# Kernel tuning notes

Hardware: AMD Instinct MI355X
Metric: run time of the kernel (lower is better)

## Reference

```python
import jax, jax.numpy as jnp
import numpy as np

N = 2_000_000   # active voxels
CIN = 16
COUT = 32
K2 = 9          # 3x3 kernel offsets


def setup_inputs() -> dict:
    key = jax.random.key(0)
    ks = jax.random.split(key, 6)
    x = jax.random.normal(ks[0], (N, CIN), dtype=jnp.float32)
    # per-offset neighbor map: nbr_idx[k, i] = input voxel feeding output i at offset k
    nbr_idx = jax.random.randint(ks[1], (K2, N), 0, N, dtype=jnp.int32)
    nbr_mask = jax.random.uniform(ks[2], (K2, N)) < 0.85
    # center offset is always the voxel itself and always valid
    nbr_idx = nbr_idx.at[K2 // 2].set(jnp.arange(N, dtype=jnp.int32))
    nbr_mask = nbr_mask.at[K2 // 2].set(True)
    s1 = 1.0 / np.sqrt(K2 * CIN)
    s2 = 1.0 / np.sqrt(K2 * COUT)
    sp = 1.0 / np.sqrt(CIN)
    W1 = jax.random.uniform(ks[3], (K2, CIN, COUT), jnp.float32, -s1, s1)
    b1 = jnp.zeros((COUT,), jnp.float32)
    W2 = jax.random.uniform(ks[4], (K2, COUT, COUT), jnp.float32, -s2, s2)
    b2 = jnp.zeros((COUT,), jnp.float32)
    Wp = jax.random.uniform(ks[5], (CIN, COUT), jnp.float32, -sp, sp)
    bp = jnp.zeros((COUT,), jnp.float32)
    return {"x": x, "W1": W1, "b1": b1, "W2": W2, "b2": b2,
            "Wp": Wp, "bp": bp, "nbr_idx": nbr_idx, "nbr_mask": nbr_mask}


def _sparse_conv(feats, W, b, nbr_idx, nbr_mask):
    """Gather-GEMM-accumulate sparse conv.
    feats: [N, Cin]; W: [K2, Cin, Cout]; nbr_idx/nbr_mask: [K2, N].
    Scans over the K2 kernel offsets so only one [N, Cin] gather lives at a time.
    """
    acc0 = jnp.zeros((feats.shape[0], W.shape[-1]), feats.dtype)

    def step(acc, kin):
        idx, m, Wk = kin
        g = feats[idx] * m[:, None].astype(feats.dtype)  # masked gather [N, Cin]
        return acc + g @ Wk, None

    acc, _ = jax.lax.scan(step, acc0, (nbr_idx, nbr_mask, W))
    return acc + b


def reference(x, W1, b1, W2, b2, Wp, bp, nbr_idx, nbr_mask):
    h = jax.nn.relu(_sparse_conv(x, W1, b1, nbr_idx, nbr_mask))
    h = _sparse_conv(h, W2, b2, nbr_idx, nbr_mask)
    identity = x @ Wp + bp  # 1x1 sparse projection (in_ch != out_ch)
    return jax.nn.relu(h + identity)
```

## Files before the change

kernel.cpp:

```cpp
#include <hip/hip_runtime.h>
#include <stdint.h>

#define CIN  16
#define COUT 32
#define K2   9

typedef __attribute__((ext_vector_type(8)))  short bf16x8;
typedef __attribute__((ext_vector_type(16))) float f32x16;
typedef __attribute__((ext_vector_type(4)))  float f32x4;

__device__ __forceinline__ uint16_t f2bf(float f) {
    union { float f; uint32_t u; } a; a.f = f;
    uint32_t u = a.u;
    uint32_t r = u + 0x7FFFu + ((u >> 16) & 1u);
    return (uint16_t)(r >> 16);
}
__device__ __forceinline__ float bf2f(uint32_t b16) {
    union { uint32_t u; float f; } a; a.u = b16 << 16; return a.f;
}

__global__ void detect_mask_kernel(const uint32_t* __restrict__ mw,
                                   int* __restrict__ flag,
                                   float* __restrict__ zrow, int n) {
    int t = threadIdx.x;
    uint32_t w = mw[(size_t)4 * (size_t)n + (size_t)t];
    unsigned long long b = __ballot(w == 1u);
    if (t == 0) *flag = (b == ~0ull) ? 1 : 0;
    if (t < 16) zrow[t] = 0.0f;
}

__device__ __forceinline__ bf16x8 make_bfrag(const float* __restrict__ W,
                                             int chbase, int col, int half) {
    bf16x8 f;
    #pragma unroll
    for (int e = 0; e < 8; ++e)
        f[e] = (short)f2bf(W[(chbase + half * 8 + e) * COUT + col]);
    return f;
}

__global__ void __launch_bounds__(256, 4)
conv1_kernel(const float* __restrict__ x,
             const float* __restrict__ W1,
             const float* __restrict__ b1,
             const int*   __restrict__ nidx,
             const void*  __restrict__ nmask,
             const int*   __restrict__ mflag,
             const char*  __restrict__ zrow,
             uint16_t*    __restrict__ hbuf,
             int n)
{
    const int lane = threadIdx.x & 63;
    const int wid  = threadIdx.x >> 6;
    const int col  = lane & 31;
    const int half = lane >> 5;
    const int mode32 = *mflag;
    const int*     m32 = (const int*)nmask;
    const uint8_t* m8  = (const uint8_t*)nmask;

    bf16x8 Bf[K2];
    #pragma unroll
    for (int k = 0; k < K2; ++k)
        Bf[k] = make_bfrag(W1 + k * (CIN * COUT), 0, col, half);
    const float bias = b1[col];

    const int ntiles = (n + 31) >> 5;
    for (int tile = blockIdx.x * 4 + wid; tile < ntiles; tile += gridDim.x * 4) {
        const int vbase = tile << 5;
        const int vr = vbase + col;
        const int vc = (vr < n) ? vr : (n - 1);

        int idv[K2];
        uint32_t mb = 0;
        #pragma unroll
        for (int k = 0; k < K2; ++k) {
            const size_t e = (size_t)k * (size_t)n + (size_t)vc;
            idv[k] = __builtin_nontemporal_load(nidx + e);
            const int m = mode32 ? (__builtin_nontemporal_load(m32 + e) != 0)
                                 : (__builtin_nontemporal_load(m8  + e) != 0);
            mb |= (uint32_t)m << k;
        }

        f32x16 acc = {};

        f32x4 xa = {}, xb = {}, xa1 = {}, xb1 = {};
        {
            const float* p = (mb & 1u)
                ? (x + (size_t)(uint32_t)idv[0] * CIN + half * 8)
                : (const float*)(zrow + half * 32);
            xa = ((const f32x4*)p)[0];
            xb = ((const f32x4*)p)[1];
        }
        #pragma unroll
        for (int k = 0; k < K2; ++k) {
            if (k + 1 < K2) {
                const float* p = ((mb >> (k + 1)) & 1u)
                    ? (x + (size_t)(uint32_t)idv[k + 1] * CIN + half * 8)
                    : (const float*)(zrow + half * 32);
                xa1 = ((const f32x4*)p)[0];
                xb1 = ((const f32x4*)p)[1];
            }
            bf16x8 hi, lo;
            #pragma unroll
            for (int e = 0; e < 8; ++e) {
                const float xv = (e < 4) ? xa[e] : xb[e - 4];
                const uint16_t hb = f2bf(xv);
                hi[e] = (short)hb;
                lo[e] = (short)f2bf(xv - bf2f(hb));
            }
            acc = __builtin_amdgcn_mfma_f32_32x32x16_bf16(hi, Bf[k], acc, 0, 0, 0);
            acc = __builtin_amdgcn_mfma_f32_32x32x16_bf16(lo, Bf[k], acc, 0, 0, 0);
            xa = xa1; xb = xb1;
        }

        #pragma unroll
        for (int r = 0; r < 16; ++r) {
            const int row = (r & 3) + 8 * (r >> 2) + 4 * half;
            const int vo = vbase + row;
            if (vo < n) {
                const float o = fmaxf(acc[r] + bias, 0.0f);
                hbuf[(size_t)vo * COUT + col] = f2bf(o);
            }
        }
    }
}

__global__ void __launch_bounds__(256, 3)
conv2_kernel(const float* __restrict__ x,
             const float* __restrict__ W2,
             const float* __restrict__ b2,
             const float* __restrict__ Wp,
             const float* __restrict__ bp,
             const int*   __restrict__ nidx,
             const void*  __restrict__ nmask,
             const int*   __restrict__ mflag,
             const char*  __restrict__ zrow,
             const uint16_t* __restrict__ hbuf,
             float*       __restrict__ out,
             int n)
{
    const int lane = threadIdx.x & 63;
    const int wid  = threadIdx.x >> 6;
    const int col  = lane & 31;
    const int half = lane >> 5;
    const int mode32 = *mflag;
    const int*     m32 = (const int*)nmask;
    const uint8_t* m8  = (const uint8_t*)nmask;

    bf16x8 Bf0[K2], Bf1[K2];
    #pragma unroll
    for (int k = 0; k < K2; ++k) {
        Bf0[k] = make_bfrag(W2 + k * (COUT * COUT), 0,  col, half);
        Bf1[k] = make_bfrag(W2 + k * (COUT * COUT), 16, col, half);
    }
    const bf16x8 Bp = make_bfrag(Wp, 0, col, half);
    const float bias = b2[col] + bp[col];

    const int ntiles = (n + 31) >> 5;
    for (int tile = blockIdx.x * 4 + wid; tile < ntiles; tile += gridDim.x * 4) {
        const int vbase = tile << 5;
        const int vr = vbase + col;
        const int vc = (vr < n) ? vr : (n - 1);

        int idv[K2];
        uint32_t mb = 0;
        #pragma unroll
        for (int k = 0; k < K2; ++k) {
            const size_t e = (size_t)k * (size_t)n + (size_t)vc;
            idv[k] = __builtin_nontemporal_load(nidx + e);
            const int m = mode32 ? (__builtin_nontemporal_load(m32 + e) != 0)
                                 : (__builtin_nontemporal_load(m8  + e) != 0);
            mb |= (uint32_t)m << k;
        }

        f32x16 acc = {};

        {
            const f32x4* xr = (const f32x4*)(x + (size_t)vc * CIN + half * 8);
            const f32x4 xa = __builtin_nontemporal_load(xr);
            const f32x4 xb = __builtin_nontemporal_load(xr + 1);
            bf16x8 hi, lo;
            #pragma unroll
            for (int e = 0; e < 8; ++e) {
                const float xv = (e < 4) ? xa[e] : xb[e - 4];
                const uint16_t hb = f2bf(xv);
                hi[e] = (short)hb;
                lo[e] = (short)f2bf(xv - bf2f(hb));
            }
            acc = __builtin_amdgcn_mfma_f32_32x32x16_bf16(hi, Bp, acc, 0, 0, 0);
            acc = __builtin_amdgcn_mfma_f32_32x32x16_bf16(lo, Bp, acc, 0, 0, 0);
        }

        bf16x8 A0, A1, N0 = {}, N1 = {};
        {
            const char* p = (mb & 1u)
                ? (const char*)hbuf + (size_t)(uint32_t)idv[0] * (COUT * 2)
                : zrow;
            A0 = *(const bf16x8*)(p + half * 16);
            A1 = *(const bf16x8*)(p + 32 + half * 16);
        }
        #pragma unroll
        for (int k = 0; k < K2; ++k) {
            if (k + 1 < K2) {
                const char* p = ((mb >> (k + 1)) & 1u)
                    ? (const char*)hbuf + (size_t)(uint32_t)idv[k + 1] * (COUT * 2)
                    : zrow;
                N0 = *(const bf16x8*)(p + half * 16);
                N1 = *(const bf16x8*)(p + 32 + half * 16);
            }
            acc = __builtin_amdgcn_mfma_f32_32x32x16_bf16(A0, Bf0[k], acc, 0, 0, 0);
            acc = __builtin_amdgcn_mfma_f32_32x32x16_bf16(A1, Bf1[k], acc, 0, 0, 0);
            A0 = N0; A1 = N1;
        }

        #pragma unroll
        for (int r = 0; r < 16; ++r) {
            const int row = (r & 3) + 8 * (r >> 2) + 4 * half;
            const int vo = vbase + row;
            if (vo < n) {
                const float o = fmaxf(acc[r] + bias, 0.0f);
                __builtin_nontemporal_store(o, out + (size_t)vo * COUT + col);
            }
        }
    }
}

extern "C" void kernel_launch(void* const* d_in, const int* in_sizes, int n_in,
                              void* d_out, int out_size, void* d_ws, size_t ws_size,
                              hipStream_t stream) {
    const float* x    = (const float*)d_in[0];
    const float* W1   = (const float*)d_in[1];
    const float* b1   = (const float*)d_in[2];
    const float* W2   = (const float*)d_in[3];
    const float* b2   = (const float*)d_in[4];
    const float* Wp   = (const float*)d_in[5];
    const float* bp   = (const float*)d_in[6];
    const int*   nidx = (const int*)d_in[7];
    const void*  nmask = d_in[8];
    const int n = in_sizes[0] / CIN;

    int*      mflag = (int*)d_ws;
    float*    zrowf = (float*)((char*)d_ws + 64);
    uint16_t* hbuf  = (uint16_t*)((char*)d_ws + 256);

    detect_mask_kernel<<<1, 64, 0, stream>>>((const uint32_t*)nmask, mflag, zrowf, n);

    const int ntiles = (n + 31) / 32;
    int grid = (ntiles + 3) / 4;
    if (grid > 1024) grid = 1024;

    conv1_kernel<<<grid, 256, 0, stream>>>(x, W1, b1, nidx, nmask, mflag,
                                           (const char*)zrowf, hbuf, n);
    conv2_kernel<<<grid, 256, 0, stream>>>(x, W2, b2, Wp, bp, nidx, nmask, mflag,
                                           (const char*)zrowf, hbuf, (float*)d_out, n);
}
```

Baseline: 1.078 ms.

## Stage weights in LDS and issue all neighbor gathers up front

Weight fragments move from per-thread registers into shared memory, converted to bf16 once per block. This frees VGPRs so conv2 can raise its occupancy bound from 3 to 4 waves, and the grid cap doubles. Both kernels now issue all nine neighbor gathers before any MFMA instead of prefetching one offset ahead, which puts more memory loads in flight to hide the latency of random gathers. The cost is an LDS read per MFMA, more registers to hold the gathered rows, and a per-block weight staging pass.

```diff
diff --git a/kernel.cpp b/kernel.cpp
--- a/kernel.cpp
+++ b/kernel.cpp
@@ -27,15 +27,6 @@
     unsigned long long b = __ballot(w == 1u);
     if (t == 0) *flag = (b == ~0ull) ? 1 : 0;
     if (t < 16) zrow[t] = 0.0f;
-}
-
-__device__ __forceinline__ bf16x8 make_bfrag(const float* __restrict__ W,
-                                             int chbase, int col, int half) {
-    bf16x8 f;
-    #pragma unroll
-    for (int e = 0; e < 8; ++e)
-        f[e] = (short)f2bf(W[(chbase + half * 8 + e) * COUT + col]);
-    return f;
 }
 
 __global__ void __launch_bounds__(256, 4)
@@ -49,6 +40,14 @@
              uint16_t*    __restrict__ hbuf,
              int n)
 {
+    __shared__ __align__(16) uint16_t smw[K2 * 2 * 32 * 8];
+
+    for (int i = threadIdx.x; i < K2 * 2 * 32 * 8; i += 256) {
+        const int e = i & 7, c2 = (i >> 3) & 31, hf = (i >> 8) & 1, k = i >> 9;
+        smw[i] = f2bf(W1[k * (CIN * COUT) + (hf * 8 + e) * COUT + c2]);
+    }
+    __syncthreads();
+
     const int lane = threadIdx.x & 63;
     const int wid  = threadIdx.x >> 6;
     const int col  = lane & 31;
@@ -57,13 +56,9 @@
     const int*     m32 = (const int*)nmask;
     const uint8_t* m8  = (const uint8_t*)nmask;
 
-    bf16x8 Bf[K2];
-    #pragma unroll
-    for (int k = 0; k < K2; ++k)
-        Bf[k] = make_bfrag(W1 + k * (CIN * COUT), 0, col, half);
     const float bias = b1[col];
-
     const int ntiles = (n + 31) >> 5;
+
     for (int tile = blockIdx.x * 4 + wid; tile < ntiles; tile += gridDim.x * 4) {
         const int vbase = tile << 5;
         const int vr = vbase + col;
@@ -80,36 +75,30 @@
             mb |= (uint32_t)m << k;
         }
 
+        f32x4 ga[K2], gb[K2];
+        #pragma unroll
+        for (int k = 0; k < K2; ++k) {
+            const float* p = ((mb >> k) & 1u)
+                ? (x + (size_t)(uint32_t)idv[k] * CIN + half * 8)
+                : (const float*)(zrow + half * 32);
+            ga[k] = ((const f32x4*)p)[0];
+            gb[k] = ((const f32x4*)p)[1];
+        }
+
         f32x16 acc = {};
-
-        f32x4 xa = {}, xb = {}, xa1 = {}, xb1 = {};
-        {
-            const float* p = (mb & 1u)
-                ? (x + (size_t)(uint32_t)idv[0] * CIN + half * 8)
-                : (const float*)(zrow + half * 32);
-            xa = ((const f32x4*)p)[0];
-            xb = ((const f32x4*)p)[1];
-        }
-        #pragma unroll
-        for (int k = 0; k < K2; ++k) {
-            if (k + 1 < K2) {
-                const float* p = ((mb >> (k + 1)) & 1u)
-                    ? (x + (size_t)(uint32_t)idv[k + 1] * CIN + half * 8)
-                    : (const float*)(zrow + half * 32);
-                xa1 = ((const f32x4*)p)[0];
-                xb1 = ((const f32x4*)p)[1];
-            }
+        #pragma unroll
+        for (int k = 0; k < K2; ++k) {
+            const bf16x8 Bf = *(const bf16x8*)&smw[((k * 2 + half) * 32 + col) * 8];
             bf16x8 hi, lo;
             #pragma unroll
             for (int e = 0; e < 8; ++e) {
-                const float xv = (e < 4) ? xa[e] : xb[e - 4];
+                const float xv = (e < 4) ? ga[k][e] : gb[k][e - 4];
                 const uint16_t hb = f2bf(xv);
                 hi[e] = (short)hb;
                 lo[e] = (short)f2bf(xv - bf2f(hb));
             }
-            acc = __builtin_amdgcn_mfma_f32_32x32x16_bf16(hi, Bf[k], acc, 0, 0, 0);
-            acc = __builtin_amdgcn_mfma_f32_32x32x16_bf16(lo, Bf[k], acc, 0, 0, 0);
-            xa = xa1; xb = xb1;
+            acc = __builtin_amdgcn_mfma_f32_32x32x16_bf16(hi, Bf, acc, 0, 0, 0);
+            acc = __builtin_amdgcn_mfma_f32_32x32x16_bf16(lo, Bf, acc, 0, 0, 0);
         }
 
         #pragma unroll
@@ -124,7 +113,7 @@
     }
 }
 
-__global__ void __launch_bounds__(256, 3)
+__global__ void __launch_bounds__(256, 4)
 conv2_kernel(const float* __restrict__ x,
              const float* __restrict__ W2,
              const float* __restrict__ b2,
@@ -138,6 +127,23 @@
              float*       __restrict__ out,
              int n)
 {
+    __shared__ __align__(16) uint16_t smw[K2 * 4 * 32 * 8 + 2 * 32 * 8];
+
+    for (int i = threadIdx.x; i < K2 * 4 * 32 * 8 + 2 * 32 * 8; i += 256) {
+        uint16_t v;
+        if (i < K2 * 4 * 32 * 8) {
+            const int e = i & 7, c2 = (i >> 3) & 31, hf = (i >> 8) & 1,
+                      cb = (i >> 9) & 1, k = i >> 10;
+            v = f2bf(W2[k * (COUT * COUT) + (cb * 16 + hf * 8 + e) * COUT + c2]);
+        } else {
+            const int j = i - K2 * 4 * 32 * 8;
+            const int e = j & 7, c2 = (j >> 3) & 31, hf = (j >> 8) & 1;
+            v = f2bf(Wp[(hf * 8 + e) * COUT + c2]);
+        }
+        smw[i] = v;
+    }
+    __syncthreads();
+
     const int lane = threadIdx.x & 63;
     const int wid  = threadIdx.x >> 6;
     const int col  = lane & 31;
@@ -146,16 +152,9 @@
     const int*     m32 = (const int*)nmask;
     const uint8_t* m8  = (const uint8_t*)nmask;
 
-    bf16x8 Bf0[K2], Bf1[K2];
-    #pragma unroll
-    for (int k = 0; k < K2; ++k) {
-        Bf0[k] = make_bfrag(W2 + k * (COUT * COUT), 0,  col, half);
-        Bf1[k] = make_bfrag(W2 + k * (COUT * COUT), 16, col, half);
-    }
-    const bf16x8 Bp = make_bfrag(Wp, 0, col, half);
     const float bias = b2[col] + bp[col];
-
     const int ntiles = (n + 31) >> 5;
+
     for (int tile = blockIdx.x * 4 + wid; tile < ntiles; tile += gridDim.x * 4) {
         const int vbase = tile << 5;
         const int vr = vbase + col;
@@ -172,12 +171,23 @@
             mb |= (uint32_t)m << k;
         }
 
+        const f32x4* xr = (const f32x4*)(x + (size_t)vc * CIN + half * 8);
+        const f32x4 xa = __builtin_nontemporal_load(xr);
+        const f32x4 xb = __builtin_nontemporal_load(xr + 1);
+
+        bf16x8 A0[K2], A1[K2];
+        #pragma unroll
+        for (int k = 0; k < K2; ++k) {
+            const char* p = ((mb >> k) & 1u)
+                ? (const char*)hbuf + (size_t)(uint32_t)idv[k] * (COUT * 2)
+                : zrow;
+            A0[k] = *(const bf16x8*)(p + half * 16);
+            A1[k] = *(const bf16x8*)(p + 32 + half * 16);
+        }
+
         f32x16 acc = {};
 
         {
-            const f32x4* xr = (const f32x4*)(x + (size_t)vc * CIN + half * 8);
-            const f32x4 xa = __builtin_nontemporal_load(xr);
-            const f32x4 xb = __builtin_nontemporal_load(xr + 1);
             bf16x8 hi, lo;
             #pragma unroll
             for (int e = 0; e < 8; ++e) {
@@ -186,30 +196,17 @@
                 hi[e] = (short)hb;
                 lo[e] = (short)f2bf(xv - bf2f(hb));
             }
+            const bf16x8 Bp = *(const bf16x8*)&smw[K2 * 4 * 32 * 8 + (half * 32 + col) * 8];
             acc = __builtin_amdgcn_mfma_f32_32x32x16_bf16(hi, Bp, acc, 0, 0, 0);
             acc = __builtin_amdgcn_mfma_f32_32x32x16_bf16(lo, Bp, acc, 0, 0, 0);
         }
 
-        bf16x8 A0, A1, N0 = {}, N1 = {};
-        {
-            const char* p = (mb & 1u)
-                ? (const char*)hbuf + (size_t)(uint32_t)idv[0] * (COUT * 2)
-                : zrow;
-            A0 = *(const bf16x8*)(p + half * 16);
-            A1 = *(const bf16x8*)(p + 32 + half * 16);
-        }
-        #pragma unroll
-        for (int k = 0; k < K2; ++k) {
-            if (k + 1 < K2) {
-                const char* p = ((mb >> (k + 1)) & 1u)
-                    ? (const char*)hbuf + (size_t)(uint32_t)idv[k + 1] * (COUT * 2)
-                    : zrow;
-                N0 = *(const bf16x8*)(p + half * 16);
-                N1 = *(const bf16x8*)(p + 32 + half * 16);
-            }
-            acc = __builtin_amdgcn_mfma_f32_32x32x16_bf16(A0, Bf0[k], acc, 0, 0, 0);
-            acc = __builtin_amdgcn_mfma_f32_32x32x16_bf16(A1, Bf1[k], acc, 0, 0, 0);
-            A0 = N0; A1 = N1;
+        #pragma unroll
+        for (int k = 0; k < K2; ++k) {
+            const bf16x8 B0 = *(const bf16x8*)&smw[(((k * 2 + 0) * 2 + half) * 32 + col) * 8];
+            const bf16x8 B1 = *(const bf16x8*)&smw[(((k * 2 + 1) * 2 + half) * 32 + col) * 8];
+            acc = __builtin_amdgcn_mfma_f32_32x32x16_bf16(A0[k], B0, acc, 0, 0, 0);
+            acc = __builtin_amdgcn_mfma_f32_32x32x16_bf16(A1[k], B1, acc, 0, 0, 0);
         }
 
         #pragma unroll
@@ -246,7 +243,7 @@
 
     const int ntiles = (n + 31) / 32;
     int grid = (ntiles + 3) / 4;
-    if (grid > 1024) grid = 1024;
+    if (grid > 2048) grid = 2048;
 
     conv1_kernel<<<grid, 256, 0, stream>>>(x, W1, b1, nidx, nmask, mflag,
                                            (const char*)zrowf, hbuf, n);
```

New measurement: 1.007 ms. 6.5% less time.
